# Kernel tuning notes

Measured on AMD Instinct MI355X. Metric: run time of the kernel, lower is better.

The kernel has to match this reference:

```python
import jax, jax.numpy as jnp
import numpy as np
from functools import partial

# ---- module hyperparameters (from init_kwargs) ----
INP_DIM = 128
OUT_DIM = 128
NOISE_LEVEL = 0.1
AB_MVM = 8   # activation bits after MVM
IB = 8       # input activation bits
WB = 8       # weight bits
BATCH = 262144


def step_d(bits):
    return 2.0 ** (bits - 1)


def pact_a(x, a):
    # PACT clip: sign(x) * 0.5 * (|x| - ||x| - a| + a)
    return jnp.sign(x) * 0.5 * (jnp.abs(x) - jnp.abs(jnp.abs(x) - a) + a)


@partial(jax.custom_vjp, nondiff_argnums=(2,))
def quant_ste(x, x_range, bits):
    # fake-quantize x to `bits` bits over [-x_range, x_range], straight-through grad
    sd = step_d(bits)
    x01 = jnp.clip(x / x_range, -1.0 + 1.0 / sd, 1.0 - 1.0 / sd)
    return jnp.round(x01 * sd) / sd * x_range


def _quant_fwd(x, x_range, bits):
    return quant_ste(x, x_range, bits), x_range


def _quant_bwd(bits, x_range, g):
    # torch QuantFunc.backward: grad passes straight through to x, None for range
    return (g, jnp.zeros_like(x_range))


quant_ste.defvjp(_quant_fwd, _quant_bwd)


def _noisy_mm(x, w, b):
    # simulated analog MVM: quantized weights + per-tensor Gaussian noise
    k1, k2 = jax.random.split(jax.random.key(1234))
    noise_w = jax.random.normal(k1, w.shape, w.dtype) * w.max() * NOISE_LEVEL
    noise_b = jax.random.normal(k2, b.shape, b.dtype) * b.max() * NOISE_LEVEL
    wq = quant_ste(w, 1.0, WB)
    bq = quant_ste(b, 1.0, WB)
    return x @ (wq + noise_w) + bq + noise_b


custom_mm = jax.custom_vjp(_noisy_mm)


def _mm_fwd(x, w, b):
    return _noisy_mm(x, w, b), (x, w)


def _mm_bwd(res, g):
    # torch CustomMM.backward uses CLEAN (un-noised, un-quantized) weight/input
    x, w = res
    return (g @ w.T, x.T @ g, g.sum(0))


custom_mm.defvjp(_mm_fwd, _mm_bwd)


def setup_inputs() -> dict:
    key = jax.random.key(0)
    kx, kw = jax.random.split(key)
    x = jax.random.normal(kx, (BATCH, INP_DIM), dtype=jnp.float32)
    # weight init: uniform(-limit, limit) with limit = max(sqrt(6/inp_dim), 1.5/2^(wb-1))
    limit = max(np.sqrt(6.0 / INP_DIM), 1.5 / (2.0 ** (WB - 1)))
    weights = jax.random.uniform(kw, (INP_DIM, OUT_DIM), dtype=jnp.float32,
                                 minval=-limit, maxval=limit)
    bias = jnp.zeros((OUT_DIM,), dtype=jnp.float32)  # torch init: uniform(0, 0)
    a1 = jnp.array([4.0], dtype=jnp.float32)
    a2 = jnp.array([16.0], dtype=jnp.float32)
    return {"x": x, "weights": weights, "bias": bias, "a1": a1, "a2": a2}


def reference(x, weights, bias, a1, a2):
    # quant_pass(pact_a(CustomMM(quant_pass(pact_a(x,a1), ib, a1), W, b, nl, wb), a2), abMVM, a2)
    xq = quant_ste(pact_a(x, a1), a1, IB)          # [B, inp_dim]
    h = custom_mm(xq, weights, bias)               # [B, out_dim]
    return quant_ste(pact_a(h, a2), a2, AB_MVM)    # [B, out_dim]
```

## Files before the change

kernel.cpp:

```cpp
#include <hip/hip_runtime.h>
#include <stdint.h>

#define INP 128
#define OUTD 128
#define WT_STRIDE 136
#define THREEFRY_PARTITIONABLE 1

typedef __bf16 bf16x8 __attribute__((ext_vector_type(8)));
typedef float  floatx4 __attribute__((ext_vector_type(4)));

__device__ __forceinline__ uint32_t rotl32(uint32_t v, uint32_t n) {
  return (v << n) | (v >> (32u - n));
}
__device__ __forceinline__ void tf_round(uint32_t& x0, uint32_t& x1, uint32_t r) {
  x0 += x1; x1 = rotl32(x1, r); x1 ^= x0;
}
__device__ void threefry2x32(uint32_t k0, uint32_t k1, uint32_t c0, uint32_t c1,
                             uint32_t& o0, uint32_t& o1) {
  uint32_t k2 = k0 ^ k1 ^ 0x1BD11BDAu;
  uint32_t x0 = c0 + k0, x1 = c1 + k1;
  tf_round(x0,x1,13); tf_round(x0,x1,15); tf_round(x0,x1,26); tf_round(x0,x1,6);
  x0 += k1; x1 += k2 + 1u;
  tf_round(x0,x1,17); tf_round(x0,x1,29); tf_round(x0,x1,16); tf_round(x0,x1,24);
  x0 += k2; x1 += k0 + 2u;
  tf_round(x0,x1,13); tf_round(x0,x1,15); tf_round(x0,x1,26); tf_round(x0,x1,6);
  x0 += k0; x1 += k1 + 3u;
  tf_round(x0,x1,17); tf_round(x0,x1,29); tf_round(x0,x1,16); tf_round(x0,x1,24);
  x0 += k1; x1 += k2 + 4u;
  tf_round(x0,x1,13); tf_round(x0,x1,15); tf_round(x0,x1,26); tf_round(x0,x1,6);
  x0 += k2; x1 += k0 + 5u;
  o0 = x0; o1 = x1;
}

__device__ float erfinv_giles(float x) {
  float w = -logf((1.0f - x) * (1.0f + x));
  float p;
  if (w < 5.0f) {
    w = w - 2.5f;
    p = 2.81022636e-08f;
    p = fmaf(p, w, 3.43273939e-07f);
    p = fmaf(p, w, -3.5233877e-06f);
    p = fmaf(p, w, -4.39150654e-06f);
    p = fmaf(p, w, 0.00021858087f);
    p = fmaf(p, w, -0.00125372503f);
    p = fmaf(p, w, -0.00417768164f);
    p = fmaf(p, w, 0.246640727f);
    p = fmaf(p, w, 1.50140941f);
  } else {
    w = sqrtf(w) - 3.0f;
    p = -0.000200214257f;
    p = fmaf(p, w, 0.000100950558f);
    p = fmaf(p, w, 0.00134934322f);
    p = fmaf(p, w, -0.00367342844f);
    p = fmaf(p, w, 0.00573950773f);
    p = fmaf(p, w, -0.0076224613f);
    p = fmaf(p, w, 0.00943887047f);
    p = fmaf(p, w, 1.00167406f);
    p = fmaf(p, w, 2.83297682f);
  }
  return p * x;
}

__device__ float normal_from_bits(uint32_t bits) {
  const float lo = -0.999999940395355224609375f;
  uint32_t fb = (bits >> 9) | 0x3F800000u;
  float f = __uint_as_float(fb) - 1.0f;
  float u = fmaxf(lo, f * 2.0f + lo);
  return 1.41421356237309515f * erfinv_giles(u);
}

__device__ __forceinline__ uint32_t rand_bits(uint32_t ka, uint32_t kb, int i, int half) {
#if THREEFRY_PARTITIONABLE
  (void)half;
  uint32_t o0, o1;
  threefry2x32(ka, kb, 0u, (uint32_t)i, o0, o1);
  return o0 ^ o1;
#else
  uint32_t c0 = (i < half) ? (uint32_t)i : (uint32_t)(i - half);
  uint32_t o0, o1;
  threefry2x32(ka, kb, c0, c0 + (uint32_t)half, o0, o1);
  return (i < half) ? o0 : o1;
#endif
}

__global__ __launch_bounds__(256) void setup_reduce(
    const float* __restrict__ w, const float* __restrict__ bias,
    float* __restrict__ biasEff, float* __restrict__ scalars) {
  __shared__ float red[8];
  const int tid = threadIdx.x;

  float m = -3.4e38f;
  for (int i = tid; i < INP * OUTD; i += 256) m = fmaxf(m, w[i]);
  #pragma unroll
  for (int off = 1; off < 64; off <<= 1) m = fmaxf(m, __shfl_xor(m, off));
  float bm = (tid < OUTD) ? bias[tid] : -3.4e38f;
  #pragma unroll
  for (int off = 1; off < 64; off <<= 1) bm = fmaxf(bm, __shfl_xor(bm, off));
  if ((tid & 63) == 0) { red[tid >> 6] = m; red[4 + (tid >> 6)] = bm; }
  __syncthreads();
  const float wmax = fmaxf(fmaxf(red[0], red[1]), fmaxf(red[2], red[3]));
  const float bmax = fmaxf(fmaxf(red[4], red[5]), fmaxf(red[6], red[7]));
  if (tid == 0) { scalars[0] = wmax; scalars[1] = bmax; }

  uint32_t k2a, k2b;
#if THREEFRY_PARTITIONABLE
  threefry2x32(0u, 1234u, 0u, 1u, k2a, k2b);
#else
  { uint32_t a0, b0, a1, b1;
    threefry2x32(0u, 1234u, 0u, 2u, a0, b0);
    threefry2x32(0u, 1234u, 1u, 3u, a1, b1);
    k2a = b0; k2b = b1; }
#endif
  if (tid < OUTD) {
    float nrm = normal_from_bits(rand_bits(k2a, k2b, tid, OUTD / 2));
    float bv = bias[tid];
    float bq = rintf(fminf(fmaxf(bv * 128.f, -127.f), 127.f)) * 0.0078125f;
    biasEff[tid] = bq + (nrm * bmax) * 0.1f;
  }
}

__global__ __launch_bounds__(256) void setup_noise(
    const float* __restrict__ w, __bf16* __restrict__ wt,
    const float* __restrict__ scalars) {
  const int i = blockIdx.x * 256 + threadIdx.x;
  const float wmax = scalars[0];

  uint32_t k1a, k1b;
#if THREEFRY_PARTITIONABLE
  threefry2x32(0u, 1234u, 0u, 0u, k1a, k1b);
#else
  { uint32_t a0, b0, a1, b1;
    threefry2x32(0u, 1234u, 0u, 2u, a0, b0);
    threefry2x32(0u, 1234u, 1u, 3u, a1, b1);
    k1a = a0; k1b = a1; }
#endif

  float nrm = normal_from_bits(rand_bits(k1a, k1b, i, (INP * OUTD) / 2));
  int r = i >> 7, c = i & 127;
  float wv = w[i];
  float wq = rintf(fminf(fmaxf(wv * 128.f, -127.f), 127.f)) * 0.0078125f;
  wt[c * WT_STRIDE + r] = (__bf16)(wq + (nrm * wmax) * 0.1f);
}

__device__ __forceinline__ void load_tile(floatx4 v[8], const float* __restrict__ x,
                                          long tile, int n16, int quad) {
  const float* p = x + ((size_t)(tile * 16 + n16) << 7) + quad * 8;
  #pragma unroll
  for (int kc = 0; kc < 4; ++kc) {
    v[2 * kc]     = *(const floatx4*)(p + kc * 32);
    v[2 * kc + 1] = *(const floatx4*)(p + kc * 32 + 4);
  }
}

__device__ __forceinline__ bf16x8 quant_pair(floatx4 v0, floatx4 v1, float s1, float r1) {
  bf16x8 a;
  #pragma unroll
  for (int i = 0; i < 4; ++i) {
    a[i]     = (__bf16)(rintf(fminf(fmaxf(v0[i] * s1, -127.f), 127.f)) * r1);
    a[i + 4] = (__bf16)(rintf(fminf(fmaxf(v1[i] * s1, -127.f), 127.f)) * r1);
  }
  return a;
}

__device__ __forceinline__ void compute_tile(
    const floatx4 v[8], const __bf16* sW, const float* sBias,
    float* __restrict__ out, long tile, int n16, int quad,
    float s1, float r1, float s2, float r2) {
  floatx4 acc[8];
  #pragma unroll
  for (int ct = 0; ct < 8; ++ct) acc[ct] = (floatx4)0.0f;

  #pragma unroll
  for (int kc = 0; kc < 4; ++kc) {
    bf16x8 a = quant_pair(v[2 * kc], v[2 * kc + 1], s1, r1);
    const int kOff = kc * 32 + quad * 8;
    #pragma unroll
    for (int ct = 0; ct < 8; ++ct) {
      bf16x8 wfrag = *(const bf16x8*)&sW[(ct * 16 + n16) * WT_STRIDE + kOff];
      acc[ct] = __builtin_amdgcn_mfma_f32_16x16x32_bf16(wfrag, a, acc[ct], 0, 0, 0);
    }
  }

  float* orow = out + ((size_t)(tile * 16 + n16) << 7);
  #pragma unroll
  for (int ct = 0; ct < 8; ++ct) {
    const int colBase = ct * 16 + quad * 4;
    floatx4 o;
    #pragma unroll
    for (int r = 0; r < 4; ++r) {
      float h = acc[ct][r] + sBias[colBase + r];
      float t = fminf(fmaxf(h * s2, -127.0f), 127.0f);
      o[r] = rintf(t) * r2;
    }
    *(floatx4*)(orow + colBase) = o;
  }
}

__global__ __launch_bounds__(256) void linlayer_main(
    const float* __restrict__ x, const __bf16* __restrict__ wt,
    const float* __restrict__ biasEff, const float* __restrict__ a1p,
    const float* __restrict__ a2p, float* __restrict__ out, int nTiles) {
  __shared__ __attribute__((aligned(16))) __bf16 sW[OUTD * WT_STRIDE];
  __shared__ float sBias[OUTD];

  const int tid  = threadIdx.x;
  const int lane = tid & 63;
  const int n16  = lane & 15;
  const int quad = lane >> 4;

  const int nWaves = gridDim.x * 4;
  const int waveId = blockIdx.x * 4 + (tid >> 6);
  const long last  = nTiles - 1;

  floatx4 bufA[8], bufB[8];
  long t = waveId;
  load_tile(bufA, x, (t <= last) ? t : last, n16, quad);

  {
    const uint4* src = (const uint4*)wt;
    uint4* dst = (uint4*)sW;
    for (int i = tid; i < (OUTD * WT_STRIDE * 2) / 16; i += 256) dst[i] = src[i];
  }
  if (tid < OUTD) sBias[tid] = biasEff[tid];

  const float a1 = a1p[0], a2 = a2p[0];
  const float s1 = 128.0f / a1, r1 = a1 * 0.0078125f;
  const float s2 = 128.0f / a2, r2 = a2 * 0.0078125f;

  __syncthreads();

  while (t <= last) {
    long tn = t + nWaves;
    load_tile(bufB, x, (tn <= last) ? tn : last, n16, quad);
    compute_tile(bufA, sW, sBias, out, t, n16, quad, s1, r1, s2, r2);
    t = tn;
    if (t > last) break;

    tn = t + nWaves;
    load_tile(bufA, x, (tn <= last) ? tn : last, n16, quad);
    compute_tile(bufB, sW, sBias, out, t, n16, quad, s1, r1, s2, r2);
    t = tn;
  }
}

extern "C" void kernel_launch(void* const* d_in, const int* in_sizes, int n_in,
                              void* d_out, int out_size, void* d_ws, size_t ws_size,
                              hipStream_t stream) {
  const float* x    = (const float*)d_in[0];
  const float* w    = (const float*)d_in[1];
  const float* bias = (const float*)d_in[2];
  const float* a1   = (const float*)d_in[3];
  const float* a2   = (const float*)d_in[4];
  float* out = (float*)d_out;

  __bf16* wt     = (__bf16*)d_ws;
  float* biasEff = (float*)((char*)d_ws + OUTD * WT_STRIDE * 2);
  float* scalars = (float*)((char*)d_ws + OUTD * WT_STRIDE * 2 + 512);

  const int rows   = in_sizes[0] / INP;
  const int nTiles = rows / 16;
  const int grid   = 1024;

  setup_reduce<<<1, 256, 0, stream>>>(w, bias, biasEff, scalars);
  setup_noise<<<64, 256, 0, stream>>>(w, wt, scalars);
  linlayer_main<<<grid, 256, 0, stream>>>(x, wt, biasEff, a1, a2, out, nTiles);
}
```

Baseline: 270.9 us.

## Load x tiles contiguously and restage through per-wave LDS for MFMA fragments

Each wave now reads its 16x128 x tile as fully contiguous 1 KB float4 rows per instruction instead of strided per-lane fragments. It writes the tile into a padded per-wave LDS buffer and reads the MFMA A fragments back from there. The aim is more coalesced global reads on this memory-bound kernel. The cost is extra LDS traffic and about 34 KB more shared memory, with the grid halved to 512 blocks. There is no barrier between the LDS write and read within a wave, so correctness depends on wave-synchronous execution.

```diff
diff --git a/kernel.cpp b/kernel.cpp
--- a/kernel.cpp
+++ b/kernel.cpp
@@ -4,6 +4,7 @@
 #define INP 128
 #define OUTD 128
 #define WT_STRIDE 136
+#define XT_STRIDE 132
 #define THREEFRY_PARTITIONABLE 1
 
 typedef __bf16 bf16x8 __attribute__((ext_vector_type(8)));
@@ -142,14 +143,20 @@
   wt[c * WT_STRIDE + r] = (__bf16)(wq + (nrm * wmax) * 0.1f);
 }
 
-__device__ __forceinline__ void load_tile(floatx4 v[8], const float* __restrict__ x,
-                                          long tile, int n16, int quad) {
-  const float* p = x + ((size_t)(tile * 16 + n16) << 7) + quad * 8;
-  #pragma unroll
-  for (int kc = 0; kc < 4; ++kc) {
-    v[2 * kc]     = *(const floatx4*)(p + kc * 32);
-    v[2 * kc + 1] = *(const floatx4*)(p + kc * 32 + 4);
-  }
+__device__ __forceinline__ void load_tile_contig(floatx4 v[8], const float* __restrict__ x,
+                                                 long tile, int lane) {
+  const float* p = x + ((size_t)tile << 11) + lane * 4;
+  #pragma unroll
+  for (int k = 0; k < 8; ++k) v[k] = *(const floatx4*)(p + k * 256);
+}
+
+__device__ __forceinline__ void stage_tile(const floatx4 v[8], float* __restrict__ myX,
+                                           int lane) {
+  const int r0 = lane >> 5;
+  const int c  = (lane & 31) * 4;
+  #pragma unroll
+  for (int k = 0; k < 8; ++k)
+    *(floatx4*)&myX[(2 * k + r0) * XT_STRIDE + c] = v[k];
 }
 
 __device__ __forceinline__ bf16x8 quant_pair(floatx4 v0, floatx4 v1, float s1, float r1) {
@@ -163,7 +170,7 @@
 }
 
 __device__ __forceinline__ void compute_tile(
-    const floatx4 v[8], const __bf16* sW, const float* sBias,
+    const float* __restrict__ myX, const __bf16* sW, const float* sBias,
     float* __restrict__ out, long tile, int n16, int quad,
     float s1, float r1, float s2, float r2) {
   floatx4 acc[8];
@@ -172,7 +179,10 @@
 
   #pragma unroll
   for (int kc = 0; kc < 4; ++kc) {
-    bf16x8 a = quant_pair(v[2 * kc], v[2 * kc + 1], s1, r1);
+    const float* fr = &myX[n16 * XT_STRIDE + kc * 32 + quad * 8];
+    floatx4 f0 = *(const floatx4*)fr;
+    floatx4 f1 = *(const floatx4*)(fr + 4);
+    bf16x8 a = quant_pair(f0, f1, s1, r1);
     const int kOff = kc * 32 + quad * 8;
     #pragma unroll
     for (int ct = 0; ct < 8; ++ct) {
@@ -201,20 +211,22 @@
     const float* __restrict__ biasEff, const float* __restrict__ a1p,
     const float* __restrict__ a2p, float* __restrict__ out, int nTiles) {
   __shared__ __attribute__((aligned(16))) __bf16 sW[OUTD * WT_STRIDE];
+  __shared__ __attribute__((aligned(16))) float sX[4][16 * XT_STRIDE];
   __shared__ float sBias[OUTD];
 
   const int tid  = threadIdx.x;
+  const int wave = tid >> 6;
   const int lane = tid & 63;
   const int n16  = lane & 15;
   const int quad = lane >> 4;
 
   const int nWaves = gridDim.x * 4;
-  const int waveId = blockIdx.x * 4 + (tid >> 6);
+  const int waveId = blockIdx.x * 4 + wave;
   const long last  = nTiles - 1;
 
   floatx4 bufA[8], bufB[8];
   long t = waveId;
-  load_tile(bufA, x, (t <= last) ? t : last, n16, quad);
+  load_tile_contig(bufA, x, (t <= last) ? t : last, lane);
 
   {
     const uint4* src = (const uint4*)wt;
@@ -229,16 +241,20 @@
 
   __syncthreads();
 
+  float* myX = sX[wave];
+
   while (t <= last) {
     long tn = t + nWaves;
-    load_tile(bufB, x, (tn <= last) ? tn : last, n16, quad);
-    compute_tile(bufA, sW, sBias, out, t, n16, quad, s1, r1, s2, r2);
+    load_tile_contig(bufB, x, (tn <= last) ? tn : last, lane);
+    stage_tile(bufA, myX, lane);
+    compute_tile(myX, sW, sBias, out, t, n16, quad, s1, r1, s2, r2);
     t = tn;
     if (t > last) break;
 
     tn = t + nWaves;
-    load_tile(bufA, x, (tn <= last) ? tn : last, n16, quad);
-    compute_tile(bufB, sW, sBias, out, t, n16, quad, s1, r1, s2, r2);
+    load_tile_contig(bufA, x, (tn <= last) ? tn : last, lane);
+    stage_tile(bufB, myX, lane);
+    compute_tile(myX, sW, sBias, out, t, n16, quad, s1, r1, s2, r2);
     t = tn;
   }
 }
@@ -259,7 +275,7 @@
 
   const int rows   = in_sizes[0] / INP;
   const int nTiles = rows / 16;
-  const int grid   = 1024;
+  const int grid   = 512;
 
   setup_reduce<<<1, 256, 0, stream>>>(w, bias, biasEff, scalars);
   setup_noise<<<64, 256, 0, stream>>>(w, wt, scalars);
```

Measured after the change: 264.6 us. -2.3%, faster.
